# Kernel tuning notes

Measured on AMD Instinct MI355X. Metric: run time of the kernel, lower is better.

Reference implementation:

```python
import jax, jax.numpy as jnp
import numpy as np

B, N, C, H, D = 1, 4096, 256, 8, 64  # batch, seq, channels, heads, head_dim


def setup_inputs() -> dict:
    key = jax.random.key(0)
    ks = jax.random.split(key, 11)
    s = 0.02
    return {
        "q_x": jax.random.normal(ks[0], (B, N, C), jnp.float32),
        "k_x": jax.random.normal(ks[1], (B, N, C), jnp.float32),
        "v_x": jax.random.normal(ks[2], (B, N, C), jnp.float32),
        "bias": jax.random.normal(ks[3], (B, 1, N, N), jnp.float32),
        "wq": jax.random.normal(ks[4], (H * D, C), jnp.float32) * s,
        "wk": jax.random.normal(ks[5], (H * D, C), jnp.float32) * s,
        "wv": jax.random.normal(ks[6], (H * D, C), jnp.float32) * s,
        "wg": jax.random.normal(ks[7], (H * D, C), jnp.float32) * s,
        "bg": jnp.ones((H * D,), jnp.float32),  # gating bias init = 1
        "wo": jax.random.normal(ks[8], (C, H * D), jnp.float32) * s,
        "bo": jnp.zeros((C,), jnp.float32),
        "q_chunk_size": 256,
        "kv_chunk_size": 1024,
    }


def reference(q_x, k_x, v_x, bias, wq, wk, wv, wg, bg, wo, bo,
              q_chunk_size, kv_chunk_size):
    # The chunked Rabe-Staats loop computes exact softmax attention; the
    # chunk sizes are memory knobs only, so the reference computes the
    # mathematically identical full attention.
    q = (q_x @ wq.T).reshape(*q_x.shape[:-1], H, D) / jnp.sqrt(jnp.asarray(D, q_x.dtype))
    k = (k_x @ wk.T).reshape(*k_x.shape[:-1], H, D)
    v = (v_x @ wv.T).reshape(*v_x.shape[:-1], H, D)
    logits = jnp.einsum("bqhd,bkhd->bhqk", q, k) + bias  # [B,H,Q,K]
    p = jax.nn.softmax(logits, axis=-1)
    o = jnp.einsum("bkhd,bhqk->bqhd", v, p)  # [B,Q,H,D]
    g = jax.nn.sigmoid(q_x @ wg.T + bg).reshape(*q_x.shape[:-1], H, D)
    o = o * g
    o = o.reshape(*o.shape[:-2], H * D)
    return o @ wo.T + bo
```

## Files before the change

kernel.cpp:

```cpp
#include <hip/hip_runtime.h>
#include <stdint.h>

#define NN 4096
#define CC 256
#define HD 512
#define DD 64
#define KSPLIT 4
#define KCHUNK (NN / KSPLIT)

typedef __attribute__((ext_vector_type(8))) short short8;
typedef __attribute__((ext_vector_type(4))) float floatx4;

__device__ __forceinline__ unsigned short f2bf(float x) {
    union { float f; unsigned int u; } v; v.f = x;
    unsigned int u = v.u + 0x7fffu + ((v.u >> 16) & 1u);
    return (unsigned short)(u >> 16);
}
__device__ __forceinline__ float bf2f(unsigned short s) {
    union { unsigned int u; float f; } v; v.u = ((unsigned int)s) << 16;
    return v.f;
}

__global__ __launch_bounds__(256) void prep_kernel(
    const float* __restrict__ qx, const float* __restrict__ kx,
    const float* __restrict__ vx,
    const float* __restrict__ wq, const float* __restrict__ wk,
    const float* __restrict__ wv, const float* __restrict__ wg,
    const float* __restrict__ wo,
    unsigned short* __restrict__ qxb, unsigned short* __restrict__ kxb,
    unsigned short* __restrict__ vxb, unsigned short* __restrict__ Wb,
    unsigned short* __restrict__ wob)
{
    const int z = blockIdx.y;
    const float* src; unsigned short* dst; int n; float s = 1.0f;
    switch (z) {
        case 0: src = qx; dst = qxb; n = NN * CC; break;
        case 1: src = kx; dst = kxb; n = NN * CC; break;
        case 2: src = vx; dst = vxb; n = NN * CC; break;
        case 3: src = wq; dst = Wb;              n = HD * CC; s = 0.125f; break;
        case 4: src = wk; dst = Wb + 1 * HD * CC; n = HD * CC; break;
        case 5: src = wv; dst = Wb + 2 * HD * CC; n = HD * CC; break;
        case 6: src = wg; dst = Wb + 3 * HD * CC; n = HD * CC; break;
        default: src = wo; dst = wob;            n = CC * HD; break;
    }
    int i = (blockIdx.x * 256 + threadIdx.x) * 4;
    if (i < n) {
        float4 v = *(const float4*)&src[i];
        ushort4 p;
        p.x = f2bf(v.x * s); p.y = f2bf(v.y * s);
        p.z = f2bf(v.z * s); p.w = f2bf(v.w * s);
        *(ushort4*)&dst[i] = p;
    }
}

__global__ __launch_bounds__(256) void proj_kernel(
    const unsigned short* __restrict__ qxb, const unsigned short* __restrict__ kxb,
    const unsigned short* __restrict__ vxb, const unsigned short* __restrict__ Wb,
    const float* __restrict__ bg,
    unsigned short* __restrict__ Qb, unsigned short* __restrict__ Kb,
    unsigned short* __restrict__ VbT, unsigned short* __restrict__ Gb)
{
    const int m0 = blockIdx.x * 128;
    const int nb = blockIdx.y;
    const int n0 = nb * 128;
    const int mode = nb >> 2;
    const unsigned short* X = (mode == 1) ? kxb : (mode == 2) ? vxb : qxb;

    const int tid = threadIdx.x;
    const int wid = tid >> 6;
    const int wr = wid >> 1, wc = wid & 1;
    const int lane = tid & 63;
    const int quad = lane >> 4;
    const int ln = lane & 15;

    __shared__ __align__(16) unsigned short smem[2 * 128 * 72];
    unsigned short* Xs = smem;
    unsigned short* Ws = smem + 128 * 72;

    floatx4 acc[4][4] = {};

    for (int k0 = 0; k0 < CC; k0 += 64) {
        #pragma unroll
        for (int i = 0; i < 4; i++) {
            int idx = i * 256 + tid;
            int r = idx >> 3, c8 = idx & 7;
            *(short8*)&Xs[r * 72 + c8 * 8] =
                *(const short8*)&X[(size_t)(m0 + r) * CC + k0 + c8 * 8];
        }
        #pragma unroll
        for (int i = 0; i < 4; i++) {
            int idx = i * 256 + tid;
            int r = idx >> 3, c8 = idx & 7;
            *(short8*)&Ws[r * 72 + c8 * 8] =
                *(const short8*)&Wb[(size_t)(n0 + r) * CC + k0 + c8 * 8];
        }
        __syncthreads();

        #pragma unroll
        for (int ks = 0; ks < 64; ks += 32) {
            short8 a[4], b[4];
            #pragma unroll
            for (int i = 0; i < 4; i++)
                a[i] = *(const short8*)&Xs[(wr * 64 + i * 16 + ln) * 72 + ks + quad * 8];
            #pragma unroll
            for (int j = 0; j < 4; j++)
                b[j] = *(const short8*)&Ws[(wc * 64 + j * 16 + ln) * 72 + ks + quad * 8];
            #pragma unroll
            for (int i = 0; i < 4; i++)
                #pragma unroll
                for (int j = 0; j < 4; j++)
                    acc[i][j] = __builtin_amdgcn_mfma_f32_16x16x32_bf16(a[i], b[j], acc[i][j], 0, 0, 0);
        }
        __syncthreads();
    }

    const int subn = nb & 3;
    if (mode != 2) {
        unsigned short* Out = (mode == 0) ? Qb : (mode == 1) ? Kb : Gb;
        #pragma unroll
        for (int i = 0; i < 4; i++) {
            #pragma unroll
            for (int j = 0; j < 4; j++) {
                int col = subn * 128 + wc * 64 + j * 16 + ln;
                float bgv = (mode == 3) ? bg[col] : 0.0f;
                #pragma unroll
                for (int r = 0; r < 4; r++) {
                    int row = m0 + wr * 64 + i * 16 + quad * 4 + r;
                    float v = acc[i][j][r];
                    if (mode == 3) v = 1.0f / (1.0f + __expf(-(v + bgv)));
                    Out[(size_t)row * HD + col] = f2bf(v);
                }
            }
        }
    } else {
        #pragma unroll
        for (int i = 0; i < 4; i++) {
            #pragma unroll
            for (int j = 0; j < 4; j++) {
                int cl = wc * 64 + j * 16 + ln;
                #pragma unroll
                for (int r = 0; r < 4; r++) {
                    int rl = wr * 64 + i * 16 + quad * 4 + r;
                    smem[cl * 136 + rl] = f2bf(acc[i][j][r]);
                }
            }
        }
        __syncthreads();
        #pragma unroll
        for (int it = 0; it < 8; it++) {
            int idx = it * 256 + tid;
            int c = idx >> 4, ch = idx & 15;
            short8 vv = *(const short8*)&smem[c * 136 + ch * 8];
            *(short8*)&VbT[(size_t)(subn * 128 + c) * NN + m0 + ch * 8] = vv;
        }
    }
}

__global__ __launch_bounds__(256) void attn_kernel(
    const unsigned short* __restrict__ Qb, const unsigned short* __restrict__ Kb,
    const unsigned short* __restrict__ VbT,
    const float* __restrict__ bias,
    unsigned short* __restrict__ Opart, float* __restrict__ Lpart)
{
    const int h = blockIdx.y;
    const int q0 = blockIdx.x * 64;
    const int sp = blockIdx.z;
    const int kbeg = sp * KCHUNK;
    const int tid = threadIdx.x;
    const int wid = tid >> 6;
    const int lane = tid & 63;
    const int quad = lane >> 4;
    const int ln = lane & 15;

    __shared__ __align__(16) unsigned short Ks[64 * 72];
    __shared__ __align__(16) unsigned short Vs[64 * 72];
    __shared__ __align__(16) unsigned short Ps[64 * 72];

    const int qrow = q0 + wid * 16 + ln;
    short8 qa0 = *(const short8*)&Qb[(size_t)qrow * HD + h * DD + quad * 8];
    short8 qa1 = *(const short8*)&Qb[(size_t)qrow * HD + h * DD + 32 + quad * 8];

    floatx4 O[4] = {};
    float lsum[4] = {0.0f, 0.0f, 0.0f, 0.0f};

    for (int k0 = kbeg; k0 < kbeg + KCHUNK; k0 += 64) {
        #pragma unroll
        for (int i = 0; i < 2; i++) {
            int idx = i * 256 + tid;
            int r = idx >> 3, c8 = idx & 7;
            *(short8*)&Ks[r * 72 + c8 * 8] =
                *(const short8*)&Kb[(size_t)(k0 + r) * HD + h * DD + c8 * 8];
        }
        #pragma unroll
        for (int i = 0; i < 2; i++) {
            int idx = i * 256 + tid;
            int d = idx >> 3, c8 = idx & 7;
            *(short8*)&Vs[d * 72 + c8 * 8] =
                *(const short8*)&VbT[(size_t)(h * DD + d) * NN + k0 + c8 * 8];
        }

        float bv[4][4];
        #pragma unroll
        for (int r = 0; r < 4; r++) {
            const float* brow = &bias[(size_t)(q0 + wid * 16 + quad * 4 + r) * NN + k0];
            #pragma unroll
            for (int n = 0; n < 4; n++) bv[r][n] = brow[n * 16 + ln];
        }
        __syncthreads();

        floatx4 S[4] = {};
        #pragma unroll
        for (int n = 0; n < 4; n++) {
            short8 b0 = *(const short8*)&Ks[(n * 16 + ln) * 72 + quad * 8];
            S[n] = __builtin_amdgcn_mfma_f32_16x16x32_bf16(qa0, b0, S[n], 0, 0, 0);
            short8 b1 = *(const short8*)&Ks[(n * 16 + ln) * 72 + 32 + quad * 8];
            S[n] = __builtin_amdgcn_mfma_f32_16x16x32_bf16(qa1, b1, S[n], 0, 0, 0);
        }

        #pragma unroll
        for (int r = 0; r < 4; r++) {
            #pragma unroll
            for (int n = 0; n < 4; n++) {
                float p = __expf(S[n][r] + bv[r][n]);
                lsum[r] += p;
                Ps[(wid * 16 + quad * 4 + r) * 72 + n * 16 + ln] = f2bf(p);
            }
        }

        #pragma unroll
        for (int ks = 0; ks < 64; ks += 32) {
            short8 a = *(const short8*)&Ps[(wid * 16 + ln) * 72 + ks + quad * 8];
            #pragma unroll
            for (int nd = 0; nd < 4; nd++) {
                short8 b = *(const short8*)&Vs[(nd * 16 + ln) * 72 + ks + quad * 8];
                O[nd] = __builtin_amdgcn_mfma_f32_16x16x32_bf16(a, b, O[nd], 0, 0, 0);
            }
        }
        __syncthreads();
    }

    #pragma unroll
    for (int r = 0; r < 4; r++) {
        #pragma unroll
        for (int off = 1; off < 16; off <<= 1)
            lsum[r] += __shfl_xor(lsum[r], off);
        int grow = q0 + wid * 16 + quad * 4 + r;
        size_t base = ((size_t)(sp * 8 + h) * NN + grow) * 64;
        #pragma unroll
        for (int nd = 0; nd < 4; nd++)
            Opart[base + nd * 16 + ln] = f2bf(O[nd][r]);
        if (ln == 0)
            Lpart[(size_t)(sp * 8 + h) * NN + grow] = lsum[r];
    }
}

__global__ __launch_bounds__(256) void combine_kernel(
    const unsigned short* __restrict__ Opart, const float* __restrict__ Lpart,
    const unsigned short* __restrict__ Gb, unsigned short* __restrict__ OGb)
{
    const int tid = threadIdx.x;
    const int d = tid & 63;
    const int flat = blockIdx.x * 4 + (tid >> 6);
    const int h = flat >> 12;
    const int q = flat & (NN - 1);

    float l = 0.0f, o = 0.0f;
    #pragma unroll
    for (int sp = 0; sp < KSPLIT; sp++) {
        size_t idx = (size_t)(sp * 8 + h) * NN + q;
        l += Lpart[idx];
        o += bf2f(Opart[idx * 64 + d]);
    }
    float inv = 1.0f / l;
    int col = h * DD + d;
    float g = bf2f(Gb[(size_t)q * HD + col]);
    OGb[(size_t)q * HD + col] = f2bf(o * inv * g);
}

__global__ __launch_bounds__(256) void outproj_kernel(
    const unsigned short* __restrict__ OGb, const unsigned short* __restrict__ wob,
    const float* __restrict__ bo, float* __restrict__ out)
{
    const int m0 = blockIdx.x * 64;
    const int n0 = blockIdx.y * 64;
    const int tid = threadIdx.x;
    const int wid = tid >> 6;
    const int lane = tid & 63;
    const int quad = lane >> 4;
    const int ln = lane & 15;

    __shared__ __align__(16) unsigned short Xs[64 * 72];
    __shared__ __align__(16) unsigned short Ws[64 * 72];

    floatx4 acc[4] = {};

    for (int k0 = 0; k0 < HD; k0 += 64) {
        #pragma unroll
        for (int i = 0; i < 2; i++) {
            int idx = i * 256 + tid;
            int r = idx >> 3, c8 = idx & 7;
            *(short8*)&Xs[r * 72 + c8 * 8] =
                *(const short8*)&OGb[(size_t)(m0 + r) * HD + k0 + c8 * 8];
        }
        #pragma unroll
        for (int i = 0; i < 2; i++) {
            int idx = i * 256 + tid;
            int r = idx >> 3, c8 = idx & 7;
            *(short8*)&Ws[r * 72 + c8 * 8] =
                *(const short8*)&wob[(size_t)(n0 + r) * HD + k0 + c8 * 8];
        }
        __syncthreads();

        #pragma unroll
        for (int ks = 0; ks < 64; ks += 32) {
            short8 a = *(const short8*)&Xs[(wid * 16 + ln) * 72 + ks + quad * 8];
            #pragma unroll
            for (int n = 0; n < 4; n++) {
                short8 b = *(const short8*)&Ws[(n * 16 + ln) * 72 + ks + quad * 8];
                acc[n] = __builtin_amdgcn_mfma_f32_16x16x32_bf16(a, b, acc[n], 0, 0, 0);
            }
        }
        __syncthreads();
    }

    #pragma unroll
    for (int n = 0; n < 4; n++) {
        int col = n0 + n * 16 + ln;
        float bov = bo[col];
        #pragma unroll
        for (int r = 0; r < 4; r++) {
            int row = m0 + wid * 16 + quad * 4 + r;
            out[(size_t)row * CC + col] = acc[n][r] + bov;
        }
    }
}

extern "C" void kernel_launch(void* const* d_in, const int* in_sizes, int n_in,
                              void* d_out, int out_size, void* d_ws, size_t ws_size,
                              hipStream_t stream) {
    const float* qx   = (const float*)d_in[0];
    const float* kx   = (const float*)d_in[1];
    const float* vx   = (const float*)d_in[2];
    const float* bias = (const float*)d_in[3];
    const float* wq   = (const float*)d_in[4];
    const float* wk   = (const float*)d_in[5];
    const float* wv   = (const float*)d_in[6];
    const float* wg   = (const float*)d_in[7];
    const float* bg   = (const float*)d_in[8];
    const float* wo   = (const float*)d_in[9];
    const float* bo   = (const float*)d_in[10];
    float* out = (float*)d_out;

    char* ws = (char*)d_ws;
    const size_t MB = (size_t)1 << 20;
    unsigned short* wob   = (unsigned short*)(ws);
    float*          Lpart = (float*)(ws + MB / 4);
    unsigned short* Qb    = (unsigned short*)(ws + 1 * MB);
    unsigned short* Kb    = (unsigned short*)(ws + 5 * MB);
    unsigned short* VbT   = (unsigned short*)(ws + 9 * MB);
    unsigned short* Gb    = (unsigned short*)(ws + 13 * MB);
    unsigned short* OGb   = (unsigned short*)(ws + 17 * MB);
    unsigned short* qxb   = (unsigned short*)(ws + 21 * MB);
    unsigned short* kxb   = (unsigned short*)(ws + 23 * MB);
    unsigned short* vxb   = (unsigned short*)(ws + 25 * MB);
    unsigned short* Wb    = (unsigned short*)(ws + 27 * MB);
    unsigned short* Opart = (unsigned short*)(ws + 21 * MB);

    prep_kernel<<<dim3(NN * CC / (256 * 4), 8), 256, 0, stream>>>(
        qx, kx, vx, wq, wk, wv, wg, wo, qxb, kxb, vxb, Wb, wob);
    proj_kernel<<<dim3(32, 16), 256, 0, stream>>>(
        qxb, kxb, vxb, Wb, bg, Qb, Kb, VbT, Gb);
    attn_kernel<<<dim3(64, 8, KSPLIT), 256, 0, stream>>>(
        Qb, Kb, VbT, bias, Opart, Lpart);
    combine_kernel<<<dim3(NN * 8 / 4), 256, 0, stream>>>(
        Opart, Lpart, Gb, OGb);
    outproj_kernel<<<dim3(64, 4), 256, 0, stream>>>(
        OGb, wob, bo, out);
}
```

Before: 231.5 us.

## Use direct global-to-LDS loads with XOR swizzle, bias-seeded MFMA, KSPLIT 3

Replaces the register-staged global→shared copies in the projection, attention and output-projection kernels with global_load_lds direct transfers into unpadded XOR-swizzled tiles. The attention kernel now folds the bias into the MFMA accumulator init, packs bf16 conversions in pairs, and splits the key range three ways instead of four, with uneven tile ranges. Launch bounds gain occupancy hints. The aim is to cut VGPR traffic, shared-memory bank conflicts and per-element conversion cost. The risks are occupancy-driven register pressure and load imbalance from the uneven split.

Result: faster. 213.6 us (-7.7%).

```diff
diff --git a/kernel.cpp b/kernel.cpp
--- a/kernel.cpp
+++ b/kernel.cpp
@@ -5,8 +5,7 @@
 #define CC 256
 #define HD 512
 #define DD 64
-#define KSPLIT 4
-#define KCHUNK (NN / KSPLIT)
+#define KSPLIT 3
 
 typedef __attribute__((ext_vector_type(8))) short short8;
 typedef __attribute__((ext_vector_type(4))) float floatx4;
@@ -20,6 +19,23 @@
     union { unsigned int u; float f; } v; v.u = ((unsigned int)s) << 16;
     return v.f;
 }
+
+#if defined(__has_builtin) && __has_builtin(__builtin_amdgcn_cvt_pk_bf16_f32)
+typedef __attribute__((ext_vector_type(2))) __bf16 bf16x2_t;
+__device__ __forceinline__ unsigned int pack2bf(float a, float b) {
+    union { bf16x2_t v; unsigned int u; } x;
+    x.v = __builtin_amdgcn_cvt_pk_bf16_f32(a, b);
+    return x.u;
+}
+#else
+__device__ __forceinline__ unsigned int pack2bf(float a, float b) {
+    return ((unsigned int)f2bf(b) << 16) | (unsigned int)f2bf(a);
+}
+#endif
+
+#define GLOAD_LDS(gp, lp) __builtin_amdgcn_global_load_lds(                    \
+    (__attribute__((address_space(1))) void*)(gp),                             \
+    (__attribute__((address_space(3))) void*)(lp), 16, 0, 0)
 
 __global__ __launch_bounds__(256) void prep_kernel(
     const float* __restrict__ qx, const float* __restrict__ kx,
@@ -37,11 +53,11 @@
         case 0: src = qx; dst = qxb; n = NN * CC; break;
         case 1: src = kx; dst = kxb; n = NN * CC; break;
         case 2: src = vx; dst = vxb; n = NN * CC; break;
-        case 3: src = wq; dst = Wb;              n = HD * CC; s = 0.125f; break;
+        case 3: src = wq; dst = Wb;               n = HD * CC; s = 0.125f; break;
         case 4: src = wk; dst = Wb + 1 * HD * CC; n = HD * CC; break;
         case 5: src = wv; dst = Wb + 2 * HD * CC; n = HD * CC; break;
         case 6: src = wg; dst = Wb + 3 * HD * CC; n = HD * CC; break;
-        default: src = wo; dst = wob;            n = CC * HD; break;
+        default: src = wo; dst = wob;             n = CC * HD; break;
     }
     int i = (blockIdx.x * 256 + threadIdx.x) * 4;
     if (i < n) {
@@ -53,7 +69,7 @@
     }
 }
 
-__global__ __launch_bounds__(256) void proj_kernel(
+__global__ __launch_bounds__(256, 4) void proj_kernel(
     const unsigned short* __restrict__ qxb, const unsigned short* __restrict__ kxb,
     const unsigned short* __restrict__ vxb, const unsigned short* __restrict__ Wb,
     const float* __restrict__ bg,
@@ -72,39 +88,38 @@
     const int lane = tid & 63;
     const int quad = lane >> 4;
     const int ln = lane & 15;
-
-    __shared__ __align__(16) unsigned short smem[2 * 128 * 72];
+    const int lnx = ln & 7;
+
+    __shared__ __align__(16) unsigned short smem[128 * 136];
     unsigned short* Xs = smem;
-    unsigned short* Ws = smem + 128 * 72;
+    unsigned short* Ws = smem + 128 * 64;
 
     floatx4 acc[4][4] = {};
 
     for (int k0 = 0; k0 < CC; k0 += 64) {
         #pragma unroll
-        for (int i = 0; i < 4; i++) {
-            int idx = i * 256 + tid;
-            int r = idx >> 3, c8 = idx & 7;
-            *(short8*)&Xs[r * 72 + c8 * 8] =
-                *(const short8*)&X[(size_t)(m0 + r) * CC + k0 + c8 * 8];
-        }
-        #pragma unroll
-        for (int i = 0; i < 4; i++) {
-            int idx = i * 256 + tid;
-            int r = idx >> 3, c8 = idx & 7;
-            *(short8*)&Ws[r * 72 + c8 * 8] =
-                *(const short8*)&Wb[(size_t)(n0 + r) * CC + k0 + c8 * 8];
+        for (int t = 0; t < 4; t++) {
+            int row = wid * 32 + t * 8 + (lane >> 3);
+            int c = (lane & 7) ^ (lane >> 3);
+            GLOAD_LDS(&X[(size_t)(m0 + row) * CC + k0 + c * 8],
+                      &Xs[(wid * 32 + t * 8) * 64]);
+            GLOAD_LDS(&Wb[(size_t)(n0 + row) * CC + k0 + c * 8],
+                      &Ws[(wid * 32 + t * 8) * 64]);
         }
         __syncthreads();
 
         #pragma unroll
         for (int ks = 0; ks < 64; ks += 32) {
+            const int cb = ks >> 3;
             short8 a[4], b[4];
             #pragma unroll
             for (int i = 0; i < 4; i++)
-                a[i] = *(const short8*)&Xs[(wr * 64 + i * 16 + ln) * 72 + ks + quad * 8];
+                a[i] = *(const short8*)&Xs[(wr * 64 + i * 16 + ln) * 64 +
+                                           (((quad ^ cb) ^ lnx) * 8)];
             #pragma unroll
             for (int j = 0; j < 4; j++)
-                b[j] = *(const short8*)&Ws[(wc * 64 + j * 16 + ln) * 72 + ks + quad * 8];
+                b[j] = *(const short8*)&Ws[(wc * 64 + j * 16 + ln) * 64 +
+                                           (((quad ^ cb) ^ lnx) * 8)];
             #pragma unroll
             for (int i = 0; i < 4; i++)
                 #pragma unroll
@@ -156,7 +171,7 @@
     }
 }
 
-__global__ __launch_bounds__(256) void attn_kernel(
+__global__ __launch_bounds__(256, 6) void attn_kernel(
     const unsigned short* __restrict__ Qb, const unsigned short* __restrict__ Kb,
     const unsigned short* __restrict__ VbT,
     const float* __restrict__ bias,
@@ -165,15 +180,17 @@
     const int h = blockIdx.y;
     const int q0 = blockIdx.x * 64;
     const int sp = blockIdx.z;
-    const int kbeg = sp * KCHUNK;
+    const int tbeg = (sp * 64) / KSPLIT;
+    const int tend = ((sp + 1) * 64) / KSPLIT;
     const int tid = threadIdx.x;
     const int wid = tid >> 6;
     const int lane = tid & 63;
     const int quad = lane >> 4;
     const int ln = lane & 15;
-
-    __shared__ __align__(16) unsigned short Ks[64 * 72];
-    __shared__ __align__(16) unsigned short Vs[64 * 72];
+    const int lnx = ln & 7;
+
+    __shared__ __align__(16) unsigned short Ks[64 * 64];
+    __shared__ __align__(16) unsigned short Vs[64 * 64];
     __shared__ __align__(16) unsigned short Ps[64 * 72];
 
     const int qrow = q0 + wid * 16 + ln;
@@ -183,20 +200,16 @@
     floatx4 O[4] = {};
     float lsum[4] = {0.0f, 0.0f, 0.0f, 0.0f};
 
-    for (int k0 = kbeg; k0 < kbeg + KCHUNK; k0 += 64) {
-        #pragma unroll
-        for (int i = 0; i < 2; i++) {
-            int idx = i * 256 + tid;
-            int r = idx >> 3, c8 = idx & 7;
-            *(short8*)&Ks[r * 72 + c8 * 8] =
-                *(const short8*)&Kb[(size_t)(k0 + r) * HD + h * DD + c8 * 8];
-        }
-        #pragma unroll
-        for (int i = 0; i < 2; i++) {
-            int idx = i * 256 + tid;
-            int d = idx >> 3, c8 = idx & 7;
-            *(short8*)&Vs[d * 72 + c8 * 8] =
-                *(const short8*)&VbT[(size_t)(h * DD + d) * NN + k0 + c8 * 8];
+    for (int kt = tbeg; kt < tend; kt++) {
+        const int k0 = kt * 64;
+        #pragma unroll
+        for (int t = 0; t < 2; t++) {
+            int row = wid * 16 + t * 8 + (lane >> 3);
+            int c = (lane & 7) ^ (lane >> 3);
+            GLOAD_LDS(&Kb[(size_t)(k0 + row) * HD + h * DD + c * 8],
+                      &Ks[(wid * 16 + t * 8) * 64]);
+            GLOAD_LDS(&VbT[(size_t)(h * DD + row) * NN + k0 + c * 8],
+                      &Vs[(wid * 16 + t * 8) * 64]);
         }
 
         float bv[4][4];
@@ -208,31 +221,40 @@
         }
         __syncthreads();
 
-        floatx4 S[4] = {};
+        floatx4 S[4];
+        #pragma unroll
+        for (int n = 0; n < 4; n++)
+            S[n] = (floatx4){bv[0][n], bv[1][n], bv[2][n], bv[3][n]};
         #pragma unroll
         for (int n = 0; n < 4; n++) {
-            short8 b0 = *(const short8*)&Ks[(n * 16 + ln) * 72 + quad * 8];
+            short8 b0 = *(const short8*)&Ks[(n * 16 + ln) * 64 + ((quad ^ lnx) * 8)];
             S[n] = __builtin_amdgcn_mfma_f32_16x16x32_bf16(qa0, b0, S[n], 0, 0, 0);
-            short8 b1 = *(const short8*)&Ks[(n * 16 + ln) * 72 + 32 + quad * 8];
+            short8 b1 = *(const short8*)&Ks[(n * 16 + ln) * 64 + (((quad ^ 4) ^ lnx) * 8)];
             S[n] = __builtin_amdgcn_mfma_f32_16x16x32_bf16(qa1, b1, S[n], 0, 0, 0);
         }
 
         #pragma unroll
         for (int r = 0; r < 4; r++) {
-            #pragma unroll
-            for (int n = 0; n < 4; n++) {
-                float p = __expf(S[n][r] + bv[r][n]);
-                lsum[r] += p;
-                Ps[(wid * 16 + quad * 4 + r) * 72 + n * 16 + ln] = f2bf(p);
+            int prow = (wid * 16 + quad * 4 + r) * 72;
+            #pragma unroll
+            for (int n = 0; n < 4; n += 2) {
+                float p0 = __expf(S[n][r]);
+                float p1 = __expf(S[n + 1][r]);
+                lsum[r] += p0 + p1;
+                unsigned int pk = pack2bf(p0, p1);
+                Ps[prow + n * 16 + ln] = (unsigned short)(pk & 0xffffu);
+                Ps[prow + (n + 1) * 16 + ln] = (unsigned short)(pk >> 16);
             }
         }
 
         #pragma unroll
         for (int ks = 0; ks < 64; ks += 32) {
+            const int cb = ks >> 3;
             short8 a = *(const short8*)&Ps[(wid * 16 + ln) * 72 + ks + quad * 8];
             #pragma unroll
             for (int nd = 0; nd < 4; nd++) {
-                short8 b = *(const short8*)&Vs[(nd * 16 + ln) * 72 + ks + quad * 8];
+                short8 b = *(const short8*)&Vs[(nd * 16 + ln) * 64 +
+                                               (((quad ^ cb) ^ lnx) * 8)];
                 O[nd] = __builtin_amdgcn_mfma_f32_16x16x32_bf16(a, b, O[nd], 0, 0, 0);
             }
         }
@@ -277,7 +299,7 @@
     OGb[(size_t)q * HD + col] = f2bf(o * inv * g);
 }
 
-__global__ __launch_bounds__(256) void outproj_kernel(
+__global__ __launch_bounds__(256, 4) void outproj_kernel(
     const unsigned short* __restrict__ OGb, const unsigned short* __restrict__ wob,
     const float* __restrict__ bo, float* __restrict__ out)
 {
@@ -288,35 +310,34 @@
     const int lane = tid & 63;
     const int quad = lane >> 4;
     const int ln = lane & 15;
-
-    __shared__ __align__(16) unsigned short Xs[64 * 72];
-    __shared__ __align__(16) unsigned short Ws[64 * 72];
+    const int lnx = ln & 7;
+
+    __shared__ __align__(16) unsigned short Xs[64 * 64];
+    __shared__ __align__(16) unsigned short Ws[64 * 64];
 
     floatx4 acc[4] = {};
 
     for (int k0 = 0; k0 < HD; k0 += 64) {
         #pragma unroll
-        for (int i = 0; i < 2; i++) {
-            int idx = i * 256 + tid;
-            int r = idx >> 3, c8 = idx & 7;
-            *(short8*)&Xs[r * 72 + c8 * 8] =
-                *(const short8*)&OGb[(size_t)(m0 + r) * HD + k0 + c8 * 8];
-        }
-        #pragma unroll
-        for (int i = 0; i < 2; i++) {
-            int idx = i * 256 + tid;
-            int r = idx >> 3, c8 = idx & 7;
-            *(short8*)&Ws[r * 72 + c8 * 8] =
-                *(const short8*)&wob[(size_t)(n0 + r) * HD + k0 + c8 * 8];
+        for (int t = 0; t < 2; t++) {
+            int row = wid * 16 + t * 8 + (lane >> 3);
+            int c = (lane & 7) ^ (lane >> 3);
+            GLOAD_LDS(&OGb[(size_t)(m0 + row) * HD + k0 + c * 8],
+                      &Xs[(wid * 16 + t * 8) * 64]);
+            GLOAD_LDS(&wob[(size_t)(n0 + row) * HD + k0 + c * 8],
+                      &Ws[(wid * 16 + t * 8) * 64]);
         }
         __syncthreads();
 
         #pragma unroll
         for (int ks = 0; ks < 64; ks += 32) {
-            short8 a = *(const short8*)&Xs[(wid * 16 + ln) * 72 + ks + quad * 8];
+            const int cb = ks >> 3;
+            short8 a = *(const short8*)&Xs[(wid * 16 + ln) * 64 +
+                                           (((quad ^ cb) ^ lnx) * 8)];
             #pragma unroll
             for (int n = 0; n < 4; n++) {
-                short8 b = *(const short8*)&Ws[(n * 16 + ln) * 72 + ks + quad * 8];
+                short8 b = *(const short8*)&Ws[(n * 16 + ln) * 64 +
+                                               (((quad ^ cb) ^ lnx) * 8)];
                 acc[n] = __builtin_amdgcn_mfma_f32_16x16x32_bf16(a, b, acc[n], 0, 0, 0);
             }
         }
```
